# Performance work log

Hardware: AMD Instinct MI355X
Metric: run time of the kernel (lower is better)

The kernel has to match this reference:

```python
import jax, jax.numpy as jnp
import numpy as np

ALPHA = 0.5
WIN_SIZE = 31
BN_EPS = 1e-5
LRELU_SLOPE = 0.1


def setup_inputs() -> dict:
    key = jax.random.key(0)
    k1, k2, k3, k4 = jax.random.split(key, 4)
    B, N, C, P, E = 4, 2048, 64, 48, 128
    return {
        "sig_new": jax.random.normal(k1, (B, N, C, P), dtype=jnp.float32),
        "atten_mem": jax.random.normal(k2, (B, N, C, P), dtype=jnp.float32),
        "conv_w": jax.random.normal(k3, (E, C, P), dtype=jnp.float32) * 0.05,
        "conv_b": jax.random.normal(k4, (E,), dtype=jnp.float32) * 0.05,
        "bn_gamma": jnp.ones((E,), dtype=jnp.float32),
        "bn_beta": jnp.zeros((E,), dtype=jnp.float32),
    }


def _neighbour_mask(n_cutout):
    # clamped banded mask (pano_scan=False / training-mode branch)
    half = WIN_SIZE // 2
    cols = jnp.clip(jnp.arange(n_cutout)[:, None] + jnp.arange(-half, half + 1)[None, :], 0, n_cutout - 1)
    rows = jnp.broadcast_to(jnp.arange(n_cutout)[:, None], cols.shape)
    return jnp.zeros((n_cutout, n_cutout), jnp.float32).at[rows, cols].set(1.0)


def _embed(x, conv_w, conv_b, bn_gamma, bn_beta, B, N):
    # Conv1d(kernel=n_pts) on length-n_pts input == full contraction over (c, p)
    y = jnp.einsum("ncp,ecp->ne", x.reshape(-1, x.shape[-2], x.shape[-1]), conv_w) + conv_b
    # BatchNorm1d, training-mode batch statistics over the (B*N) batch dim
    mu = y.mean(axis=0)
    var = ((y - mu) ** 2).mean(axis=0)
    y = (y - mu) * jax.lax.rsqrt(var + BN_EPS) * bn_gamma + bn_beta
    y = jnp.where(y >= 0, y, LRELU_SLOPE * y)  # LeakyReLU(0.1)
    return y.reshape(B, N, -1)


def reference(sig_new, atten_mem, conv_w, conv_b, bn_gamma, bn_beta):
    B, N, C, P = sig_new.shape
    mask = _neighbour_mask(N)
    embed_x = _embed(sig_new, conv_w, conv_b, bn_gamma, bn_beta, B, N)      # [B,N,E]
    embed_t = _embed(atten_mem, conv_w, conv_b, bn_gamma, bn_beta, B, N)    # [B,N,E]
    sim = jnp.einsum("bie,bje->bij", embed_x, embed_t)                      # [B,N,N]
    sim = sim - 1e10 * (1.0 - mask)
    mx = jnp.max(sim, axis=-1, keepdims=True)
    ex = jnp.exp(sim - mx) * mask
    attn = ex / jnp.sum(ex, axis=-1, keepdims=True)                          # [B,N,N]
    mem_flat = atten_mem.reshape(B, N, C * P)
    mem_w = jnp.einsum("bij,bjf->bif", attn, mem_flat).reshape(B, N, C, P)
    new_mem = ALPHA * sig_new + (1.0 - ALPHA) * mem_w
    return new_mem, attn
```

## Files before the change

### kernel.cpp

```cpp
#include <hip/hip_runtime.h>

#define BATCH 4
#define NDIM 2048
#define EDIM 128
#define KDIM 3072
#define MDIM 8192
#define HALF 15

typedef __attribute__((ext_vector_type(8))) short short8v;
typedef __attribute__((ext_vector_type(4))) float f32x4;

__device__ inline ushort bf16h(float x) {
  union { float f; unsigned u; } v; v.f = x;
  unsigned r = v.u + 0x7fff + ((v.u >> 16) & 1);
  return (ushort)(r >> 16);
}
__device__ inline float bf2f(ushort h) {
  union { unsigned u; float f; } v; v.u = ((unsigned)h) << 16;
  return v.f;
}

#define BMT 128
#define BK 32

__global__ __launch_bounds__(256, 2)
void k_gemm(const float* __restrict__ x0, const float* __restrict__ x1,
            const float* __restrict__ w, float* __restrict__ part, int splitK) {
  const int tid = threadIdx.x;
  const int m0 = blockIdx.x * BMT;
  const int kc = blockIdx.y;
  const int inp = blockIdx.z;
  const float* __restrict__ x = inp ? x1 : x0;
  const int kpc = KDIM / splitK;
  const int kbeg = kc * kpc;
  const int nsteps = kpc / BK;

  __shared__ ushort sAh[BMT][BK];
  __shared__ ushort sAl[BMT][BK];
  __shared__ ushort sBh[EDIM][BK];
  __shared__ ushort sBl[EDIM][BK];

  const int mrow = tid >> 3;
  const int c4 = (tid & 7) << 2;

  const int lane = tid & 63;
  const int wid = tid >> 6;
  const int wr = wid >> 1;
  const int wc = wid & 1;
  const int fr = lane & 15;
  const int kg = (lane >> 4) << 3;

  f32x4 acc[4][4];
#pragma unroll
  for (int a = 0; a < 4; ++a)
#pragma unroll
    for (int b = 0; b < 4; ++b) acc[a][b] = (f32x4){0.f, 0.f, 0.f, 0.f};

  float4 rA[4], rB[4];
  {
    const float* xb = x + (size_t)(m0 + mrow) * KDIM + kbeg + c4;
    const float* wb = w + (size_t)mrow * KDIM + kbeg + c4;
#pragma unroll
    for (int i = 0; i < 4; ++i) {
      rA[i] = *(const float4*)(xb + (size_t)(32 * i) * KDIM);
      rB[i] = *(const float4*)(wb + (size_t)(32 * i) * KDIM);
    }
  }

  for (int st = 0; st < nsteps; ++st) {
    __syncthreads();
#pragma unroll
    for (int i = 0; i < 4; ++i) {
      const int m = mrow + 32 * i;
      const float fa[4] = {rA[i].x, rA[i].y, rA[i].z, rA[i].w};
      const float fb[4] = {rB[i].x, rB[i].y, rB[i].z, rB[i].w};
      ushort4 ah, al, bh, bl;
      ushort* pah = (ushort*)&ah; ushort* pal = (ushort*)&al;
      ushort* pbh = (ushort*)&bh; ushort* pbl = (ushort*)&bl;
#pragma unroll
      for (int j = 0; j < 4; ++j) {
        ushort h = bf16h(fa[j]); pah[j] = h; pal[j] = bf16h(fa[j] - bf2f(h));
        ushort g = bf16h(fb[j]); pbh[j] = g; pbl[j] = bf16h(fb[j] - bf2f(g));
      }
      *(ushort4*)&sAh[m][c4] = ah;
      *(ushort4*)&sAl[m][c4] = al;
      *(ushort4*)&sBh[m][c4] = bh;
      *(ushort4*)&sBl[m][c4] = bl;
    }
    __syncthreads();

    if (st + 1 < nsteps) {
      const int ko = kbeg + (st + 1) * BK + c4;
      const float* xb = x + (size_t)(m0 + mrow) * KDIM + ko;
      const float* wb = w + (size_t)mrow * KDIM + ko;
#pragma unroll
      for (int i = 0; i < 4; ++i) {
        rA[i] = *(const float4*)(xb + (size_t)(32 * i) * KDIM);
        rB[i] = *(const float4*)(wb + (size_t)(32 * i) * KDIM);
      }
    }

    short8v ah[4], al[4], bh[4], bl[4];
#pragma unroll
    for (int mi = 0; mi < 4; ++mi) {
      const int row = wr * 64 + mi * 16 + fr;
      ah[mi] = *(const short8v*)&sAh[row][kg];
      al[mi] = *(const short8v*)&sAl[row][kg];
    }
#pragma unroll
    for (int ei = 0; ei < 4; ++ei) {
      const int e = wc * 64 + ei * 16 + fr;
      bh[ei] = *(const short8v*)&sBh[e][kg];
      bl[ei] = *(const short8v*)&sBl[e][kg];
    }
#pragma unroll
    for (int mi = 0; mi < 4; ++mi)
#pragma unroll
      for (int ei = 0; ei < 4; ++ei) {
        acc[mi][ei] = __builtin_amdgcn_mfma_f32_16x16x32_bf16(ah[mi], bh[ei], acc[mi][ei], 0, 0, 0);
        acc[mi][ei] = __builtin_amdgcn_mfma_f32_16x16x32_bf16(ah[mi], bl[ei], acc[mi][ei], 0, 0, 0);
        acc[mi][ei] = __builtin_amdgcn_mfma_f32_16x16x32_bf16(al[mi], bh[ei], acc[mi][ei], 0, 0, 0);
      }
  }

  float* po = part + ((size_t)(inp * splitK + kc) * MDIM + m0) * EDIM;
#pragma unroll
  for (int mi = 0; mi < 4; ++mi) {
    const int mloc = wr * 64 + mi * 16 + ((lane >> 4) << 2);
#pragma unroll
    for (int ei = 0; ei < 4; ++ei) {
      const int e = wc * 64 + ei * 16 + fr;
#pragma unroll
      for (int r = 0; r < 4; ++r)
        po[(size_t)(mloc + r) * EDIM + e] = acc[mi][ei][r];
    }
  }
}

__global__ __launch_bounds__(256)
void k_reduce(const float* __restrict__ part, const float* __restrict__ bvec,
              float* __restrict__ y, float* __restrict__ spart, int splitK) {
  const int tid = threadIdx.x;
  const int in = blockIdx.z;
  const int rb = blockIdx.x;
  const int e = tid & 127;
  const int rh = tid >> 7;
  const float bb = bvec[e];
  float s = 0.f, s2 = 0.f;
  for (int rr = 0; rr < 32; ++rr) {
    const int r = rb * 64 + rh * 32 + rr;
    float v = 0.f;
    for (int kc = 0; kc < splitK; ++kc)
      v += part[((size_t)(in * splitK + kc) * MDIM + r) * EDIM + e];
    v += bb;
    y[((size_t)in * MDIM + r) * EDIM + e] = v;
    s += v; s2 += v * v;
  }
  __shared__ float l1[256], l2[256];
  l1[tid] = s; l2[tid] = s2;
  __syncthreads();
  if (rh == 0) {
    s = l1[e] + l1[e + 128];
    s2 = l2[e] + l2[e + 128];
    spart[((size_t)(in * 128 + rb) * 2 + 0) * 128 + e] = s;
    spart[((size_t)(in * 128 + rb) * 2 + 1) * 128 + e] = s2;
  }
}

__global__ void k_finalize(const float* __restrict__ spart, const float* __restrict__ gamma,
                           const float* __restrict__ beta, float* __restrict__ scsh) {
  const int in = blockIdx.x;
  const int e = threadIdx.x;
  float s = 0.f, s2 = 0.f;
  for (int rb = 0; rb < 128; ++rb) {
    s  += spart[((size_t)(in * 128 + rb) * 2 + 0) * 128 + e];
    s2 += spart[((size_t)(in * 128 + rb) * 2 + 1) * 128 + e];
  }
  const float mu = s * (1.f / MDIM);
  const float var = s2 * (1.f / MDIM) - mu * mu;
  const float rs = rsqrtf(var + 1e-5f);
  const float sc = gamma[e] * rs;
  const float sh = beta[e] - mu * sc;
  scsh[in * 128 + e] = sc;
  scsh[256 + in * 128 + e] = sh;
}

__global__ __launch_bounds__(256)
void k_bnapply(float* __restrict__ y, const float* __restrict__ scsh) {
  int q = blockIdx.x * 256 + threadIdx.x;
  float4* yv = (float4*)y;
#pragma unroll
  for (int it = 0; it < 2; ++it, q += 262144) {
    float4 v = yv[q];
    const int in = q >> 18;
    const int e0 = (q & 31) << 2;
    const float* sc = scsh + in * 128 + e0;
    const float* sh = scsh + 256 + in * 128 + e0;
    float t;
    t = fmaf(sc[0], v.x, sh[0]); v.x = t >= 0.f ? t : 0.1f * t;
    t = fmaf(sc[1], v.y, sh[1]); v.y = t >= 0.f ? t : 0.1f * t;
    t = fmaf(sc[2], v.z, sh[2]); v.z = t >= 0.f ? t : 0.1f * t;
    t = fmaf(sc[3], v.w, sh[3]); v.w = t >= 0.f ? t : 0.1f * t;
    yv[q] = v;
  }
}

__global__ __launch_bounds__(256)
void k_sim(const float* __restrict__ y, float* __restrict__ attn, float* __restrict__ aw) {
  const int tid = threadIdx.x;
  const int row = blockIdx.x * 4 + (tid >> 6);
  const int lane = tid & 63;
  const int b = row >> 11;
  const int i = row & 2047;
  const int jlo = max(0, i - HALF);
  const int jhi = min(NDIM - 1, i + HALF);
  const int j = jlo + lane;
  const bool valid = (lane < 31) && (j <= jhi);
  const int jc = valid ? j : jlo;
  const float* __restrict__ xr = y + (size_t)row * EDIM;
  const float* __restrict__ tr = y + (size_t)MDIM * EDIM + ((size_t)(b << 11) + jc) * EDIM;
  float s = 0.f;
#pragma unroll
  for (int e = 0; e < EDIM; e += 4) {
    float4 u = *(const float4*)(xr + e);
    float4 v = *(const float4*)(tr + e);
    s = fmaf(u.x, v.x, s); s = fmaf(u.y, v.y, s);
    s = fmaf(u.z, v.z, s); s = fmaf(u.w, v.w, s);
  }
  float sm = valid ? s : -1e30f;
  float mx = sm;
#pragma unroll
  for (int o = 1; o < 64; o <<= 1) mx = fmaxf(mx, __shfl_xor(mx, o));
  const float p = valid ? __expf(sm - mx) : 0.f;
  float ss = p;
#pragma unroll
  for (int o = 1; o < 64; o <<= 1) ss += __shfl_xor(ss, o);
  const float a = p / ss;
  if (valid) attn[(size_t)row * NDIM + j] = a;
  if (lane < 32) aw[(size_t)row * 32 + lane] = valid ? a : 0.f;
}

#define TI 16
#define TJMAX 46
#define FC 256

__global__ __launch_bounds__(256, 2)
void k_memw(const float* __restrict__ sig, const float* __restrict__ mem,
            const float* __restrict__ aw, float* __restrict__ out) {
  const int tid = threadIdx.x;
  const int fc0 = blockIdx.x * FC;
  const int i0 = blockIdx.y * TI;
  const int b = blockIdx.z;
  const int jlo = max(0, i0 - HALF);
  const int jhi = min(NDIM - 1, i0 + TI - 1 + HALF);
  const int tj = jhi - jlo + 1;

  __shared__ float sV[TJMAX][FC];
  __shared__ float sWt[TJMAX][TI];

  for (int idx = tid; idx < tj * TI; idx += 256) {
    const int jj = idx >> 4;
    const int ii = idx & 15;
    const int ii_g = i0 + ii;
    const int jg = jlo + jj;
    const int jli = max(0, ii_g - HALF);
    const int jhii = min(NDIM - 1, ii_g + HALF);
    float wv = 0.f;
    if (jg >= jli && jg <= jhii) wv = aw[(size_t)((b << 11) + ii_g) * 32 + (jg - jli)];
    sWt[jj][ii] = wv;
  }
  for (int idx = tid; idx < tj * (FC / 4); idx += 256) {
    const int jj = idx >> 6;
    const int f4 = idx & 63;
    *(float4*)&sV[jj][f4 << 2] =
        *(const float4*)(mem + (size_t)((b << 11) + jlo + jj) * KDIM + fc0 + (f4 << 2));
  }
  __syncthreads();

  const int ig = tid >> 6;
  const int fg = tid & 63;
  const int ibase = i0 + (ig << 2);
  const int wlo = max(jlo, ibase - HALF) - jlo;
  const int whi = min(jhi, ibase + 3 + HALF) - jlo;

  float acc[4][4];
#pragma unroll
  for (int a = 0; a < 4; ++a)
#pragma unroll
    for (int c = 0; c < 4; ++c) acc[a][c] = 0.f;

  for (int jj = wlo; jj <= whi; ++jj) {
    float4 wv = *(const float4*)&sWt[jj][ig << 2];
    float4 vv = *(const float4*)&sV[jj][fg << 2];
    const float wa[4] = {wv.x, wv.y, wv.z, wv.w};
    const float va[4] = {vv.x, vv.y, vv.z, vv.w};
#pragma unroll
    for (int mi = 0; mi < 4; ++mi)
#pragma unroll
      for (int fi = 0; fi < 4; ++fi)
        acc[mi][fi] = fmaf(wa[mi], va[fi], acc[mi][fi]);
  }

  const size_t base = (size_t)((b << 11) + ibase) * KDIM + fc0 + (fg << 2);
#pragma unroll
  for (int mi = 0; mi < 4; ++mi) {
    float4 sv = *(const float4*)(sig + base + (size_t)mi * KDIM);
    float4 ov;
    ov.x = 0.5f * sv.x + 0.5f * acc[mi][0];
    ov.y = 0.5f * sv.y + 0.5f * acc[mi][1];
    ov.z = 0.5f * sv.z + 0.5f * acc[mi][2];
    ov.w = 0.5f * sv.w + 0.5f * acc[mi][3];
    *(float4*)(out + base + (size_t)mi * KDIM) = ov;
  }
}

extern "C" void kernel_launch(void* const* d_in, const int* in_sizes, int n_in,
                              void* d_out, int out_size, void* d_ws, size_t ws_size,
                              hipStream_t stream) {
  const float* sig   = (const float*)d_in[0];
  const float* mem   = (const float*)d_in[1];
  const float* w     = (const float*)d_in[2];
  const float* bv    = (const float*)d_in[3];
  const float* gamma = (const float*)d_in[4];
  const float* beta  = (const float*)d_in[5];

  float* out_mem  = (float*)d_out;
  float* out_attn = out_mem + (size_t)BATCH * NDIM * KDIM;

  float* wsf = (float*)d_ws;
  const size_t ME = (size_t)MDIM * EDIM;
  const size_t fixed = 2 * ME + 65536 + 512 + 262144;
  int splitK = 4;
  while (splitK > 1 && ((size_t)2 * splitK * ME + fixed) * 4 > ws_size) splitK >>= 1;

  float* part  = wsf;
  float* y     = part + (size_t)2 * splitK * ME;
  float* spart = y + 2 * ME;
  float* scsh  = spart + 65536;
  float* aw    = scsh + 512;

  hipMemsetAsync(out_attn, 0, (size_t)BATCH * NDIM * NDIM * sizeof(float), stream);

  dim3 g1(MDIM / BMT, splitK, 2);
  hipLaunchKernelGGL(k_gemm, g1, dim3(256), 0, stream, sig, mem, w, part, splitK);

  dim3 g2(MDIM / 64, 1, 2);
  hipLaunchKernelGGL(k_reduce, g2, dim3(256), 0, stream, part, bv, y, spart, splitK);

  hipLaunchKernelGGL(k_finalize, dim3(2), dim3(128), 0, stream, spart, gamma, beta, scsh);

  hipLaunchKernelGGL(k_bnapply, dim3(1024), dim3(256), 0, stream, y, scsh);

  hipLaunchKernelGGL(k_sim, dim3(MDIM / 4), dim3(256), 0, stream, y, out_attn, aw);

  dim3 g6(KDIM / FC, NDIM / TI, BATCH);
  hipLaunchKernelGGL(k_memw, g6, dim3(256), 0, stream, sig, mem, aw, out_mem);
}
```

Before: 475.0 us.

## Pre-split weights to bf16 hi/lo, fuse attn zero-fill into softmax, raise splitK

A new prep kernel splits conv weights into bf16 high and low halves once per call, so the GEMM no longer reconverts the shared weight tile in every block, and the high half becomes plain truncation. The separate memset of the dense attention matrix is removed; the softmax kernel now writes each full row, zeros included, with float4 stores, which drops one full pass over the 64 MB output. splitK is raised from 4 to 8 to expose more blocks, at the cost of larger partial buffers and more reduction work. Using truncation for the high half changes rounding slightly, but the low half carries the residual.

Measured after the change: 527.2 us. 1.11x slower.

```diff
diff --git a/kernel.cpp b/kernel.cpp
--- a/kernel.cpp
+++ b/kernel.cpp
@@ -15,9 +15,22 @@
   unsigned r = v.u + 0x7fff + ((v.u >> 16) & 1);
   return (ushort)(r >> 16);
 }
-__device__ inline float bf2f(ushort h) {
-  union { unsigned u; float f; } v; v.u = ((unsigned)h) << 16;
-  return v.f;
+
+__global__ __launch_bounds__(256)
+void k_wprep(const float* __restrict__ w, ushort* __restrict__ wh, ushort* __restrict__ wl) {
+  const int q = (blockIdx.x * 256 + threadIdx.x) * 4;
+  float4 v = *(const float4*)(w + q);
+  const float f[4] = {v.x, v.y, v.z, v.w};
+  ushort4 h, l;
+  ushort* ph = (ushort*)&h; ushort* pl = (ushort*)&l;
+#pragma unroll
+  for (int j = 0; j < 4; ++j) {
+    unsigned u = __float_as_uint(f[j]);
+    ph[j] = (ushort)(u >> 16);
+    pl[j] = bf16h(f[j] - __uint_as_float(u & 0xffff0000u));
+  }
+  *(ushort4*)(wh + q) = h;
+  *(ushort4*)(wl + q) = l;
 }
 
 #define BMT 128
@@ -25,7 +38,8 @@
 
 __global__ __launch_bounds__(256, 2)
 void k_gemm(const float* __restrict__ x0, const float* __restrict__ x1,
-            const float* __restrict__ w, float* __restrict__ part, int splitK) {
+            const ushort* __restrict__ wh, const ushort* __restrict__ wl,
+            float* __restrict__ part, int splitK) {
   const int tid = threadIdx.x;
   const int m0 = blockIdx.x * BMT;
   const int kc = blockIdx.y;
@@ -56,14 +70,17 @@
 #pragma unroll
     for (int b = 0; b < 4; ++b) acc[a][b] = (f32x4){0.f, 0.f, 0.f, 0.f};
 
-  float4 rA[4], rB[4];
+  float4 rA[4];
+  ushort4 rBh[4], rBl[4];
   {
     const float* xb = x + (size_t)(m0 + mrow) * KDIM + kbeg + c4;
-    const float* wb = w + (size_t)mrow * KDIM + kbeg + c4;
+    const ushort* wb = wh + (size_t)mrow * KDIM + kbeg + c4;
+    const ushort* wb2 = wl + (size_t)mrow * KDIM + kbeg + c4;
 #pragma unroll
     for (int i = 0; i < 4; ++i) {
-      rA[i] = *(const float4*)(xb + (size_t)(32 * i) * KDIM);
-      rB[i] = *(const float4*)(wb + (size_t)(32 * i) * KDIM);
+      rA[i]  = *(const float4*)(xb + (size_t)(32 * i) * KDIM);
+      rBh[i] = *(const ushort4*)(wb + (size_t)(32 * i) * KDIM);
+      rBl[i] = *(const ushort4*)(wb2 + (size_t)(32 * i) * KDIM);
     }
   }
 
@@ -73,30 +90,31 @@
     for (int i = 0; i < 4; ++i) {
       const int m = mrow + 32 * i;
       const float fa[4] = {rA[i].x, rA[i].y, rA[i].z, rA[i].w};
-      const float fb[4] = {rB[i].x, rB[i].y, rB[i].z, rB[i].w};
-      ushort4 ah, al, bh, bl;
+      ushort4 ah, al;
       ushort* pah = (ushort*)&ah; ushort* pal = (ushort*)&al;
-      ushort* pbh = (ushort*)&bh; ushort* pbl = (ushort*)&bl;
 #pragma unroll
       for (int j = 0; j < 4; ++j) {
-        ushort h = bf16h(fa[j]); pah[j] = h; pal[j] = bf16h(fa[j] - bf2f(h));
-        ushort g = bf16h(fb[j]); pbh[j] = g; pbl[j] = bf16h(fb[j] - bf2f(g));
+        unsigned u = __float_as_uint(fa[j]);
+        pah[j] = (ushort)(u >> 16);
+        pal[j] = bf16h(fa[j] - __uint_as_float(u & 0xffff0000u));
       }
       *(ushort4*)&sAh[m][c4] = ah;
       *(ushort4*)&sAl[m][c4] = al;
-      *(ushort4*)&sBh[m][c4] = bh;
-      *(ushort4*)&sBl[m][c4] = bl;
+      *(ushort4*)&sBh[m][c4] = rBh[i];
+      *(ushort4*)&sBl[m][c4] = rBl[i];
     }
     __syncthreads();
 
     if (st + 1 < nsteps) {
       const int ko = kbeg + (st + 1) * BK + c4;
       const float* xb = x + (size_t)(m0 + mrow) * KDIM + ko;
-      const float* wb = w + (size_t)mrow * KDIM + ko;
+      const ushort* wb = wh + (size_t)mrow * KDIM + ko;
+      const ushort* wb2 = wl + (size_t)mrow * KDIM + ko;
 #pragma unroll
       for (int i = 0; i < 4; ++i) {
-        rA[i] = *(const float4*)(xb + (size_t)(32 * i) * KDIM);
-        rB[i] = *(const float4*)(wb + (size_t)(32 * i) * KDIM);
+        rA[i]  = *(const float4*)(xb + (size_t)(32 * i) * KDIM);
+        rBh[i] = *(const ushort4*)(wb + (size_t)(32 * i) * KDIM);
+        rBl[i] = *(const ushort4*)(wb2 + (size_t)(32 * i) * KDIM);
       }
     }
 
@@ -236,7 +254,20 @@
 #pragma unroll
   for (int o = 1; o < 64; o <<= 1) ss += __shfl_xor(ss, o);
   const float a = p / ss;
-  if (valid) attn[(size_t)row * NDIM + j] = a;
+
+  float* orow = attn + (size_t)row * NDIM;
+  const int bw = jhi - jlo;
+  for (int c0 = lane << 2; c0 < NDIM; c0 += 256) {
+    float4 v;
+    float* pv = (float*)&v;
+#pragma unroll
+    for (int t = 0; t < 4; ++t) {
+      const int d = c0 + t - jlo;
+      const float val = __shfl(a, d & 63);
+      pv[t] = (d >= 0 && d <= bw) ? val : 0.f;
+    }
+    *(float4*)(orow + c0) = v;
+  }
   if (lane < 32) aw[(size_t)row * 32 + lane] = valid ? a : 0.f;
 }
 
@@ -329,8 +360,8 @@
 
   float* wsf = (float*)d_ws;
   const size_t ME = (size_t)MDIM * EDIM;
-  const size_t fixed = 2 * ME + 65536 + 512 + 262144;
-  int splitK = 4;
+  const size_t fixed = 2 * ME + 65536 + 512 + 262144 + 196608;
+  int splitK = 8;
   while (splitK > 1 && ((size_t)2 * splitK * ME + fixed) * 4 > ws_size) splitK >>= 1;
 
   float* part  = wsf;
@@ -338,11 +369,13 @@
   float* spart = y + 2 * ME;
   float* scsh  = spart + 65536;
   float* aw    = scsh + 512;
-
-  hipMemsetAsync(out_attn, 0, (size_t)BATCH * NDIM * NDIM * sizeof(float), stream);
+  ushort* wh   = (ushort*)(aw + 262144);
+  ushort* wl   = wh + (size_t)EDIM * KDIM;
+
+  hipLaunchKernelGGL(k_wprep, dim3(EDIM * KDIM / 1024), dim3(256), 0, stream, w, wh, wl);
 
   dim3 g1(MDIM / BMT, splitK, 2);
-  hipLaunchKernelGGL(k_gemm, g1, dim3(256), 0, stream, sig, mem, w, part, splitK);
+  hipLaunchKernelGGL(k_gemm, g1, dim3(256), 0, stream, sig, mem, wh, wl, part, splitK);
 
   dim3 g2(MDIM / 64, 1, 2);
   hipLaunchKernelGGL(k_reduce, g2, dim3(256), 0, stream, part, bv, y, spart, splitK);
```
